# Kernel tuning notes

Hardware: AMD Instinct MI355X
Metric: run time of the kernel (lower is better)

The kernel has to match this reference:

```python
import jax, jax.numpy as jnp
import numpy as np

N = 50000   # nodes
E = 800000  # edges
D = 256     # input_dim == hidden_dim (required by original code path)
O = 32      # output_dim
ALPHA = 0.5      # APPNP teleport
ALPHA_RES = 0.0  # residual mix on output
BETA = 1.0       # neighbor-aggregation scale
EPS = 1e-12


def _l2norm(h):
    # F.normalize(h, p=2, dim=1)
    n = jnp.sqrt(jnp.sum(h * h, axis=1, keepdims=True))
    return h / jnp.maximum(n, EPS)


def _gappnp(x, row, col):
    # GAPPNP with K=1, symmetric normalization, self-loops (APPNP-style step)
    sl = jnp.arange(N, dtype=row.dtype)
    r = jnp.concatenate([row, sl])
    c = jnp.concatenate([col, sl])
    deg = jax.ops.segment_sum(jnp.ones(r.shape, x.dtype), r, num_segments=N)
    dinv = jnp.where(deg > 0, jax.lax.rsqrt(jnp.maximum(deg, 1.0)), 0.0)
    norm = dinv[r] * dinv[c]                      # [E+N]
    agg = jax.ops.segment_sum(norm[:, None] * x[c], r, num_segments=N)  # [N, D]
    h = (1.0 - ALPHA) * BETA * agg + ALPHA * x
    return (1.0 - ALPHA_RES) * h + ALPHA_RES * x


def setup_inputs() -> dict:
    key = jax.random.key(0)
    ks = jax.random.split(key, 8)
    s = 1.0 / np.sqrt(D)
    return {
        "x": jax.random.normal(ks[0], (N, D), dtype=jnp.float32),
        "edge_index": jax.random.randint(ks[1], (2, E), 0, N, dtype=jnp.int32),
        "W0": jax.random.normal(ks[2], (D, D), dtype=jnp.float32) * s,
        "b0": jnp.zeros((D,), jnp.float32),
        "Wn0": jax.random.normal(ks[3], (D, D), dtype=jnp.float32) * s,
        "bn0": jnp.zeros((D,), jnp.float32),
        "W1": jax.random.normal(ks[4], (D, D), dtype=jnp.float32) * s,
        "b1": jnp.zeros((D,), jnp.float32),
        "Wn1": jax.random.normal(ks[5], (D, D), dtype=jnp.float32) * s,
        "bn1": jnp.zeros((D,), jnp.float32),
        "W2": jax.random.normal(ks[6], (D, O), dtype=jnp.float32) * s,
        "b2": jnp.zeros((O,), jnp.float32),
    }


def reference(x, edge_index, W0, b0, Wn0, bn0, W1, b1, Wn1, bn1, W2, b2):
    # eval mode: dropout is identity
    row, col = edge_index[0], edge_index[1]
    h = x
    for (W, b, Wn, bn) in ((W0, b0, Wn0, bn0), (W1, b1, Wn1, bn1)):
        h = h @ W + b                       # fc[c]
        nb = h @ Wn + bn                    # fc_n[c] (separate_neighbors)
        nb = _gappnp(nb, row, col)          # propagate neighbors
        h = h + nb
        h = _l2norm(h)                      # norm == 'normalize'
        h = jax.nn.relu(h)                  # activation 'relu'
    h = h @ W2 + b2                         # final layer, no norm (c != 0)
    return h
```

## Files before the change

kernel.cpp:

```cpp
#include <hip/hip_runtime.h>
#include <hip/hip_bf16.h>

#define NN 50000
#define NE 800000
#define DD 256
#define OO 32
#define EB 3125
#define CASTB 12500
#define BCAP 64

typedef __attribute__((ext_vector_type(8))) short short8;
typedef __attribute__((ext_vector_type(4))) float float4v;

#define AS1 __attribute__((address_space(1)))
#define AS3 __attribute__((address_space(3)))

__device__ __forceinline__ float lo16f(unsigned int u) {
    union { unsigned int i; float f; } x; x.i = u << 16; return x.f;
}
__device__ __forceinline__ float hi16f(unsigned int u) {
    union { unsigned int i; float f; } x; x.i = u & 0xFFFF0000u; return x.f;
}
__device__ __forceinline__ unsigned short f2b(float f) {
    union { float f; unsigned int i; } x;
    x.f = f;
    unsigned int r = x.i + 0x7FFFu + ((x.i >> 16) & 1u);
    return (unsigned short)(r >> 16);
}

__device__ __forceinline__ int pack_idx(int k, int n) {
    return (k >> 5) * 8192 + (n >> 4) * 512 + (((k & 31) >> 3) * 16 + (n & 15)) * 8 + (k & 7);
}

__global__ __launch_bounds__(256) void pre_all(const int* __restrict__ row,
                                               const int* __restrict__ col,
                                               int* __restrict__ cnt,
                                               unsigned short* __restrict__ bucket,
                                               const float* __restrict__ x,
                                               unsigned short* __restrict__ xb,
                                               const float* __restrict__ W0,
                                               const float* __restrict__ Wn0,
                                               const float* __restrict__ W1,
                                               const float* __restrict__ Wn1,
                                               const float* __restrict__ W2,
                                               const float* __restrict__ b0_,
                                               const float* __restrict__ bn0,
                                               const float* __restrict__ b1_,
                                               const float* __restrict__ bn1,
                                               unsigned short* __restrict__ Wp0,
                                               unsigned short* __restrict__ Wp1,
                                               unsigned short* __restrict__ Wt2,
                                               float* __restrict__ bc0,
                                               float* __restrict__ bc1) {
    __shared__ float wrow[256];
    int b = blockIdx.x, t = threadIdx.x;
    if (b < EB) {
        int e = b * 256 + t;
        int r = row[e], c = col[e];
        int p = atomicAdd(&cnt[r], 1);
        if (p < BCAP) bucket[(size_t)r * BCAP + p] = (unsigned short)c;
    } else if (b < EB + 256) {
        int n = b - EB;
        Wp0[pack_idx(t, n)] = f2b(W0[t * 256 + n]);
    } else if (b < EB + 512) {
        int n = b - (EB + 256);
        Wp1[pack_idx(t, n)] = f2b(W1[t * 256 + n]);
    } else if (b < EB + 544) {
        int n = b - (EB + 512);
        Wt2[n * 256 + t] = f2b(W2[t * 32 + n]);
    } else if (b < EB + 800) {
        int k = b - (EB + 544);
        wrow[t] = W0[k * 256 + t];
        __syncthreads();
        float s = 0.f;
#pragma unroll 8
        for (int m = 0; m < 256; ++m) s = fmaf(wrow[m], Wn0[m * 256 + t], s);
        Wp0[pack_idx(k + 256, t)] = f2b(s);
    } else if (b < EB + 1056) {
        int k = b - (EB + 800);
        wrow[t] = W1[k * 256 + t];
        __syncthreads();
        float s = 0.f;
#pragma unroll 8
        for (int m = 0; m < 256; ++m) s = fmaf(wrow[m], Wn1[m * 256 + t], s);
        Wp1[pack_idx(k + 256, t)] = f2b(s);
    } else if (b == EB + 1056) {
        float s0 = bn0[t], s1 = bn1[t];
        for (int m = 0; m < 256; ++m) {
            s0 = fmaf(b0_[m], Wn0[m * 256 + t], s0);
            s1 = fmaf(b1_[m], Wn1[m * 256 + t], s1);
        }
        bc0[t] = s0;
        bc1[t] = s1;
    } else {
        int i = (b - (EB + 1057)) * 256 + t;
        float4 v = ((const float4*)x)[i];
        ushort4 o;
        o.x = f2b(v.x); o.y = f2b(v.y); o.z = f2b(v.z); o.w = f2b(v.w);
        ((ushort4*)xb)[i] = o;
    }
}

__global__ __launch_bounds__(256) void agg_g(const unsigned short* __restrict__ A,
                                             const int* __restrict__ cnt,
                                             const unsigned short* __restrict__ bucket,
                                             unsigned short* __restrict__ G,
                                             float* __restrict__ pv) {
    int wave = threadIdx.x >> 6, lane = threadIdx.x & 63;
    int half = lane >> 5, s = lane & 31;
    int v = blockIdx.x * 4 + wave;
    const uint4* A4 = (const uint4*)A;

    int deg = cnt[v];
    float dv = rsqrtf((float)(deg + 1));
    if (deg > BCAP) deg = BCAP;

    int c = 0;
    float dc = 0.f;
    if (lane < deg) {
        c = bucket[(size_t)v * BCAP + lane];
        dc = rsqrtf((float)(cnt[c] + 1));
    }
    float sdc = dc;

    float a0 = 0.f, a1 = 0.f, a2 = 0.f, a3 = 0.f;
    float a4 = 0.f, a5 = 0.f, a6 = 0.f, a7 = 0.f;

    int pairs4 = (((deg + 1) >> 1) + 3) & ~3;
    for (int j = 0; j < pairs4; j += 4) {
        int ci[4];
        float di[4];
        uint4 u[4];
#pragma unroll
        for (int q = 0; q < 4; ++q) {
            int srcl = 2 * (j + q) + half;
            ci[q] = __shfl(c, srcl);
            di[q] = __shfl(dc, srcl);
        }
#pragma unroll
        for (int q = 0; q < 4; ++q) u[q] = A4[(size_t)ci[q] * 32 + s];
#pragma unroll
        for (int q = 0; q < 4; ++q) {
            a0 = fmaf(di[q], lo16f(u[q].x), a0);
            a1 = fmaf(di[q], hi16f(u[q].x), a1);
            a2 = fmaf(di[q], lo16f(u[q].y), a2);
            a3 = fmaf(di[q], hi16f(u[q].y), a3);
            a4 = fmaf(di[q], lo16f(u[q].z), a4);
            a5 = fmaf(di[q], hi16f(u[q].z), a5);
            a6 = fmaf(di[q], lo16f(u[q].w), a6);
            a7 = fmaf(di[q], hi16f(u[q].w), a7);
        }
    }

    a0 += __shfl_xor(a0, 32); a1 += __shfl_xor(a1, 32);
    a2 += __shfl_xor(a2, 32); a3 += __shfl_xor(a3, 32);
    a4 += __shfl_xor(a4, 32); a5 += __shfl_xor(a5, 32);
    a6 += __shfl_xor(a6, 32); a7 += __shfl_xor(a7, 32);
#pragma unroll
    for (int o = 32; o > 0; o >>= 1) sdc += __shfl_xor(sdc, o);

    if (half == 0) {
        uint4 au = A4[(size_t)v * 32 + s];
        float av[8] = {lo16f(au.x), hi16f(au.x), lo16f(au.y), hi16f(au.y),
                       lo16f(au.z), hi16f(au.z), lo16f(au.w), hi16f(au.w)};
        float aa[8] = {a0, a1, a2, a3, a4, a5, a6, a7};
        unsigned short ov[8];
#pragma unroll
        for (int i = 0; i < 8; ++i)
            ov[i] = f2b(0.5f * dv * (dv * av[i] + aa[i]) + 0.5f * av[i]);
        *(short8*)&G[(size_t)v * 256 + s * 8] = *(short8*)ov;
    }
    if (lane == 0) pv[v] = 0.5f * dv * (dv + sdc) + 0.5f;
}

__global__ __launch_bounds__(256, 2) void gemm512_norm(const unsigned short* __restrict__ A,
                                                       const unsigned short* __restrict__ G,
                                                       const unsigned short* __restrict__ Wp,
                                                       const float* __restrict__ bias,
                                                       const float* __restrict__ biasc,
                                                       const float* __restrict__ pv,
                                                       unsigned short* __restrict__ Out,
                                                       int M) {
    __shared__ unsigned short smem[16384];
    int tid = threadIdx.x, lane = tid & 63, wave = tid >> 6;
    int fr = lane & 15, quad = lane >> 4, fk = quad * 8;
    int rb = blockIdx.x * 128;

    int r0 = rb + wave * 32 + fr;      if (r0 >= M) r0 = M - 1;
    int r1 = rb + wave * 32 + 16 + fr; if (r1 >= M) r1 = M - 1;
    const unsigned short* ap0 = A + (size_t)r0 * 256 + fk;
    const unsigned short* ap1 = A + (size_t)r1 * 256 + fk;
    const unsigned short* gp0 = G + (size_t)r0 * 256 + fk;
    const unsigned short* gp1 = G + (size_t)r1 * 256 + fk;

    float4v acc[2][16];
#pragma unroll
    for (int i = 0; i < 2; ++i)
#pragma unroll
        for (int j = 0; j < 16; ++j) acc[i][j] = (float4v){0.f, 0.f, 0.f, 0.f};

#pragma unroll
    for (int i = 0; i < 4; ++i) {
        int ch = wave * 4 + i;
        __builtin_amdgcn_global_load_lds((const AS1 void*)(Wp + ch * 512 + lane * 8),
                                         (AS3 void*)&smem[ch * 512], 16, 0, 0);
    }
    short8 a0c = *(const short8*)ap0;
    short8 a1c = *(const short8*)ap1;

    for (int kk = 0; kk < 16; ++kk) {
        __syncthreads();
        int cur = (kk & 1) * 8192;
        if (kk < 15) {
            int nxt = ((kk + 1) & 1) * 8192;
#pragma unroll
            for (int i = 0; i < 4; ++i) {
                int ch = wave * 4 + i;
                __builtin_amdgcn_global_load_lds(
                    (const AS1 void*)(Wp + (kk + 1) * 8192 + ch * 512 + lane * 8),
                    (AS3 void*)&smem[nxt + ch * 512], 16, 0, 0);
            }
        }
        short8 a0n, a1n;
        if (kk < 15) {
            int kn = kk + 1;
            a0n = (kn < 8) ? *(const short8*)(ap0 + kn * 32) : *(const short8*)(gp0 + (kn - 8) * 32);
            a1n = (kn < 8) ? *(const short8*)(ap1 + kn * 32) : *(const short8*)(gp1 + (kn - 8) * 32);
        }
#pragma unroll
        for (int j = 0; j < 16; ++j) {
            short8 b = *(const short8*)&smem[cur + j * 512 + lane * 8];
            acc[0][j] = __builtin_amdgcn_mfma_f32_16x16x32_bf16(a0c, b, acc[0][j], 0, 0, 0);
            acc[1][j] = __builtin_amdgcn_mfma_f32_16x16x32_bf16(a1c, b, acc[1][j], 0, 0, 0);
        }
        a0c = a0n;
        a1c = a1n;
    }

    float bv[16], bcv[16];
#pragma unroll
    for (int j = 0; j < 16; ++j) {
        bv[j] = bias[j * 16 + fr];
        bcv[j] = biasc[j * 16 + fr];
    }
    float pvr[2][4];
#pragma unroll
    for (int i = 0; i < 2; ++i)
#pragma unroll
        for (int r = 0; r < 4; ++r) {
            int rg = rb + wave * 32 + i * 16 + quad * 4 + r;
            if (rg >= M) rg = M - 1;
            pvr[i][r] = pv[rg];
        }
    float ss[2][4] = {{0.f, 0.f, 0.f, 0.f}, {0.f, 0.f, 0.f, 0.f}};
#pragma unroll
    for (int i = 0; i < 2; ++i)
#pragma unroll
        for (int j = 0; j < 16; ++j)
#pragma unroll
            for (int r = 0; r < 4; ++r) {
                float t = acc[i][j][r] + bv[j] + pvr[i][r] * bcv[j];
                acc[i][j][r] = t;
                ss[i][r] = fmaf(t, t, ss[i][r]);
            }
#pragma unroll
    for (int o = 1; o < 16; o <<= 1)
#pragma unroll
        for (int i = 0; i < 2; ++i)
#pragma unroll
            for (int r = 0; r < 4; ++r) ss[i][r] += __shfl_xor(ss[i][r], o);
    float inv[2][4];
#pragma unroll
    for (int i = 0; i < 2; ++i)
#pragma unroll
        for (int r = 0; r < 4; ++r) inv[i][r] = 1.0f / fmaxf(sqrtf(ss[i][r]), 1e-12f);

#pragma unroll
    for (int rd = 0; rd < 2; ++rd) {
        __syncthreads();
        if ((wave >> 1) == rd) {
#pragma unroll
            for (int i = 0; i < 2; ++i)
#pragma unroll
                for (int j = 0; j < 16; ++j)
#pragma unroll
                    for (int r = 0; r < 4; ++r)
                        smem[((wave & 1) * 32 + i * 16 + quad * 4 + r) * 256 + j * 16 + fr] =
                            f2b(fmaxf(acc[i][j][r] * inv[i][r], 0.f));
        }
        __syncthreads();
#pragma unroll
        for (int b = 0; b < 8; ++b) {
            int chunk = b * 256 + tid;
            int rw = chunk >> 5, part = chunk & 31;
            int gr = rb + rd * 64 + rw;
            if (gr < M)
                *(short8*)&Out[(size_t)gr * 256 + part * 8] =
                    *(const short8*)&smem[rw * 256 + part * 8];
        }
    }
}

__global__ __launch_bounds__(256) void gemm_final_mfma(const unsigned short* __restrict__ A,
                                                       const unsigned short* __restrict__ Wt2,
                                                       const float* __restrict__ b2,
                                                       float* __restrict__ out, int M) {
    __shared__ unsigned short Als[128 * 32];
    __shared__ unsigned short Bls[32 * 32];
    int tid = threadIdx.x;
    int lane = tid & 63, wave = tid >> 6;
    int rowBase = blockIdx.x * 128;

    float4v acc[2][2];
#pragma unroll
    for (int i = 0; i < 2; ++i)
#pragma unroll
        for (int j = 0; j < 2; ++j) acc[i][j] = (float4v){0.f, 0.f, 0.f, 0.f};

    int sRow = wave * 32 + (lane >> 2);
    int sK = (lane & 3) * 8;
    int fr = lane & 15, fk = (lane >> 4) * 8;
    int bn = tid >> 3, bk4 = (tid & 7) * 4;

    for (int k0 = 0; k0 < 256; k0 += 32) {
        int r0 = rowBase + sRow;       if (r0 >= M) r0 = M - 1;
        int r1 = rowBase + sRow + 16;  if (r1 >= M) r1 = M - 1;
        __builtin_amdgcn_global_load_lds((const AS1 void*)(A + (size_t)r0 * 256 + k0 + sK),
                                         (AS3 void*)&Als[(wave * 32) * 32], 16, 0, 0);
        __builtin_amdgcn_global_load_lds((const AS1 void*)(A + (size_t)r1 * 256 + k0 + sK),
                                         (AS3 void*)&Als[(wave * 32 + 16) * 32], 16, 0, 0);
        *(ushort4*)&Bls[bn * 32 + bk4] = *(const ushort4*)&Wt2[bn * 256 + k0 + bk4];
        __syncthreads();

        short8 af[2], bfr[2];
#pragma unroll
        for (int i = 0; i < 2; ++i)
            af[i] = *(const short8*)&Als[(wave * 32 + i * 16 + fr) * 32 + fk];
#pragma unroll
        for (int j = 0; j < 2; ++j)
            bfr[j] = *(const short8*)&Bls[(j * 16 + fr) * 32 + fk];
#pragma unroll
        for (int i = 0; i < 2; ++i)
#pragma unroll
            for (int j = 0; j < 2; ++j)
                acc[i][j] = __builtin_amdgcn_mfma_f32_16x16x32_bf16(af[i], bfr[j], acc[i][j], 0, 0, 0);
        __syncthreads();
    }

    int cr = (lane >> 4) * 4, cc = lane & 15;
#pragma unroll
    for (int i = 0; i < 2; ++i) {
#pragma unroll
        for (int j = 0; j < 2; ++j) {
            int colg = j * 16 + cc;
            float bv = b2[colg];
#pragma unroll
            for (int r = 0; r < 4; ++r) {
                int rowg = rowBase + wave * 32 + i * 16 + cr + r;
                if (rowg < M) out[(size_t)rowg * 32 + colg] = acc[i][j][r] + bv;
            }
        }
    }
}

extern "C" void kernel_launch(void* const* d_in, const int* in_sizes, int n_in,
                              void* d_out, int out_size, void* d_ws, size_t ws_size,
                              hipStream_t stream) {
    const float* x   = (const float*)d_in[0];
    const int* edge  = (const int*)d_in[1];
    const float* W0  = (const float*)d_in[2];
    const float* b0  = (const float*)d_in[3];
    const float* Wn0 = (const float*)d_in[4];
    const float* bn0 = (const float*)d_in[5];
    const float* W1  = (const float*)d_in[6];
    const float* b1  = (const float*)d_in[7];
    const float* Wn1 = (const float*)d_in[8];
    const float* bn1 = (const float*)d_in[9];
    const float* W2  = (const float*)d_in[10];
    const float* b2  = (const float*)d_in[11];
    float* out = (float*)d_out;

    const int N = NN, E = NE;
    const int* row = edge;
    const int* col = edge + E;

    char* p = (char*)d_ws;
    unsigned short* Xbf = (unsigned short*)p; p += (size_t)N * DD * 2;
    unsigned short* Gbf = (unsigned short*)p; p += (size_t)N * DD * 2;
    unsigned short* Abf = (unsigned short*)p; p += (size_t)N * DD * 2;
    unsigned short* Wp0 = (unsigned short*)p; p += 16 * 8192 * 2;
    unsigned short* Wp1 = (unsigned short*)p; p += 16 * 8192 * 2;
    unsigned short* Wt2 = (unsigned short*)p; p += 32 * 256 * 2;
    float* bc0   = (float*)p; p += 256 * 4;
    float* bc1   = (float*)p; p += 256 * 4;
    float* pv    = (float*)p; p += (size_t)N * 4;
    int* cnt     = (int*)p; p += (size_t)N * 4;
    unsigned short* bucket = (unsigned short*)p; p += (size_t)N * BCAP * 2;

    hipMemsetAsync(cnt, 0, (size_t)N * sizeof(int), stream);

    pre_all<<<EB + 1057 + CASTB, 256, 0, stream>>>(row, col, cnt, bucket, x, Xbf,
                                                   W0, Wn0, W1, Wn1, W2,
                                                   b0, bn0, b1, bn1,
                                                   Wp0, Wp1, Wt2, bc0, bc1);

    const int gTiles = (N + 127) / 128;
    agg_g<<<N / 4, 256, 0, stream>>>(Xbf, cnt, bucket, Gbf, pv);
    gemm512_norm<<<gTiles, 256, 0, stream>>>(Xbf, Gbf, Wp0, b0, bc0, pv, Abf, N);
    agg_g<<<N / 4, 256, 0, stream>>>(Abf, cnt, bucket, Gbf, pv);
    gemm512_norm<<<gTiles, 256, 0, stream>>>(Abf, Gbf, Wp1, b1, bc1, pv, Xbf, N);
    gemm_final_mfma<<<(N + 127) / 128, 256, 0, stream>>>(Xbf, Wt2, b2, out, N);
}
```

Measured before the change: 325.2 us.

## Fuse final output projection into second GEMM epilogue; vectorize edge bucketing

The final 256x32 projection is computed inside the second gemm512_norm epilogue. It uses the normalized tile already held in shared memory plus a swizzled LDS copy of Wt2, so the layer-2 activations are never written to and reread from global memory and one kernel launch is dropped. The edge-bucketing blocks now each process two edges per thread using int2 loads, which halves that block count. The cost is extra LDS use (16 KB for Wt2) and more epilogue work in the templated kernel, which could reduce occupancy.

```diff
diff --git a/kernel.cpp b/kernel.cpp
--- a/kernel.cpp
+++ b/kernel.cpp
@@ -5,7 +5,7 @@
 #define NE 800000
 #define DD 256
 #define OO 32
-#define EB 3125
+#define EB2 1563
 #define CASTB 12500
 #define BCAP 64
 
@@ -54,37 +54,42 @@
                                                float* __restrict__ bc1) {
     __shared__ float wrow[256];
     int b = blockIdx.x, t = threadIdx.x;
-    if (b < EB) {
-        int e = b * 256 + t;
-        int r = row[e], c = col[e];
-        int p = atomicAdd(&cnt[r], 1);
-        if (p < BCAP) bucket[(size_t)r * BCAP + p] = (unsigned short)c;
-    } else if (b < EB + 256) {
-        int n = b - EB;
+    if (b < EB2) {
+        int i = b * 256 + t;
+        if (i < NE / 2) {
+            int2 r2 = ((const int2*)row)[i];
+            int2 c2 = ((const int2*)col)[i];
+            int p0 = atomicAdd(&cnt[r2.x], 1);
+            if (p0 < BCAP) bucket[(size_t)r2.x * BCAP + p0] = (unsigned short)c2.x;
+            int p1 = atomicAdd(&cnt[r2.y], 1);
+            if (p1 < BCAP) bucket[(size_t)r2.y * BCAP + p1] = (unsigned short)c2.y;
+        }
+    } else if (b < EB2 + 256) {
+        int n = b - EB2;
         Wp0[pack_idx(t, n)] = f2b(W0[t * 256 + n]);
-    } else if (b < EB + 512) {
-        int n = b - (EB + 256);
+    } else if (b < EB2 + 512) {
+        int n = b - (EB2 + 256);
         Wp1[pack_idx(t, n)] = f2b(W1[t * 256 + n]);
-    } else if (b < EB + 544) {
-        int n = b - (EB + 512);
+    } else if (b < EB2 + 544) {
+        int n = b - (EB2 + 512);
         Wt2[n * 256 + t] = f2b(W2[t * 32 + n]);
-    } else if (b < EB + 800) {
-        int k = b - (EB + 544);
+    } else if (b < EB2 + 800) {
+        int k = b - (EB2 + 544);
         wrow[t] = W0[k * 256 + t];
         __syncthreads();
         float s = 0.f;
 #pragma unroll 8
         for (int m = 0; m < 256; ++m) s = fmaf(wrow[m], Wn0[m * 256 + t], s);
         Wp0[pack_idx(k + 256, t)] = f2b(s);
-    } else if (b < EB + 1056) {
-        int k = b - (EB + 800);
+    } else if (b < EB2 + 1056) {
+        int k = b - (EB2 + 800);
         wrow[t] = W1[k * 256 + t];
         __syncthreads();
         float s = 0.f;
 #pragma unroll 8
         for (int m = 0; m < 256; ++m) s = fmaf(wrow[m], Wn1[m * 256 + t], s);
         Wp1[pack_idx(k + 256, t)] = f2b(s);
-    } else if (b == EB + 1056) {
+    } else if (b == EB2 + 1056) {
         float s0 = bn0[t], s1 = bn1[t];
         for (int m = 0; m < 256; ++m) {
             s0 = fmaf(b0_[m], Wn0[m * 256 + t], s0);
@@ -93,7 +98,7 @@
         bc0[t] = s0;
         bc1[t] = s1;
     } else {
-        int i = (b - (EB + 1057)) * 256 + t;
+        int i = (b - (EB2 + 1057)) * 256 + t;
         float4 v = ((const float4*)x)[i];
         ushort4 o;
         o.x = f2b(v.x); o.y = f2b(v.y); o.z = f2b(v.z); o.w = f2b(v.w);
@@ -173,6 +178,7 @@
     if (lane == 0) pv[v] = 0.5f * dv * (dv + sdc) + 0.5f;
 }
 
+template <int FINAL>
 __global__ __launch_bounds__(256, 2) void gemm512_norm(const unsigned short* __restrict__ A,
                                                        const unsigned short* __restrict__ G,
                                                        const unsigned short* __restrict__ Wp,
@@ -180,8 +186,12 @@
                                                        const float* __restrict__ biasc,
                                                        const float* __restrict__ pv,
                                                        unsigned short* __restrict__ Out,
+                                                       const unsigned short* __restrict__ Wt2,
+                                                       const float* __restrict__ b2,
+                                                       float* __restrict__ outF,
                                                        int M) {
     __shared__ unsigned short smem[16384];
+    __shared__ unsigned short wt2ls[FINAL ? 8192 : 16];
     int tid = threadIdx.x, lane = tid & 63, wave = tid >> 6;
     int fr = lane & 15, quad = lane >> 4, fk = quad * 8;
     int rb = blockIdx.x * 128;
@@ -237,6 +247,16 @@
         a1c = a1n;
     }
 
+    if (FINAL) {
+#pragma unroll
+        for (int c = 0; c < 4; ++c) {
+            int idx = tid * 4 + c;
+            int n = idx >> 5, ch = idx & 31;
+            *(short8*)&wt2ls[n * 256 + ((ch ^ (n & 7)) << 3)] =
+                *(const short8*)&Wt2[n * 256 + ch * 8];
+        }
+    }
+
     float bv[16], bcv[16];
 #pragma unroll
     for (int j = 0; j < 16; ++j) {
@@ -284,80 +304,53 @@
 #pragma unroll
                 for (int j = 0; j < 16; ++j)
 #pragma unroll
-                    for (int r = 0; r < 4; ++r)
-                        smem[((wave & 1) * 32 + i * 16 + quad * 4 + r) * 256 + j * 16 + fr] =
-                            f2b(fmaxf(acc[i][j][r] * inv[i][r], 0.f));
+                    for (int r = 0; r < 4; ++r) {
+                        int rw = (wave & 1) * 32 + i * 16 + quad * 4 + r;
+                        unsigned short hv = f2b(fmaxf(acc[i][j][r] * inv[i][r], 0.f));
+                        if (FINAL) {
+                            int e = j * 16 + fr;
+                            smem[rw * 256 + (((e >> 3) ^ (rw & 7)) << 3) + (e & 7)] = hv;
+                        } else {
+                            smem[rw * 256 + j * 16 + fr] = hv;
+                        }
+                    }
         }
         __syncthreads();
-#pragma unroll
-        for (int b = 0; b < 8; ++b) {
-            int chunk = b * 256 + tid;
-            int rw = chunk >> 5, part = chunk & 31;
-            int gr = rb + rd * 64 + rw;
-            if (gr < M)
-                *(short8*)&Out[(size_t)gr * 256 + part * 8] =
-                    *(const short8*)&smem[rw * 256 + part * 8];
-        }
-    }
-}
-
-__global__ __launch_bounds__(256) void gemm_final_mfma(const unsigned short* __restrict__ A,
-                                                       const unsigned short* __restrict__ Wt2,
-                                                       const float* __restrict__ b2,
-                                                       float* __restrict__ out, int M) {
-    __shared__ unsigned short Als[128 * 32];
-    __shared__ unsigned short Bls[32 * 32];
-    int tid = threadIdx.x;
-    int lane = tid & 63, wave = tid >> 6;
-    int rowBase = blockIdx.x * 128;
-
-    float4v acc[2][2];
-#pragma unroll
-    for (int i = 0; i < 2; ++i)
-#pragma unroll
-        for (int j = 0; j < 2; ++j) acc[i][j] = (float4v){0.f, 0.f, 0.f, 0.f};
-
-    int sRow = wave * 32 + (lane >> 2);
-    int sK = (lane & 3) * 8;
-    int fr = lane & 15, fk = (lane >> 4) * 8;
-    int bn = tid >> 3, bk4 = (tid & 7) * 4;
-
-    for (int k0 = 0; k0 < 256; k0 += 32) {
-        int r0 = rowBase + sRow;       if (r0 >= M) r0 = M - 1;
-        int r1 = rowBase + sRow + 16;  if (r1 >= M) r1 = M - 1;
-        __builtin_amdgcn_global_load_lds((const AS1 void*)(A + (size_t)r0 * 256 + k0 + sK),
-                                         (AS3 void*)&Als[(wave * 32) * 32], 16, 0, 0);
-        __builtin_amdgcn_global_load_lds((const AS1 void*)(A + (size_t)r1 * 256 + k0 + sK),
-                                         (AS3 void*)&Als[(wave * 32 + 16) * 32], 16, 0, 0);
-        *(ushort4*)&Bls[bn * 32 + bk4] = *(const ushort4*)&Wt2[bn * 256 + k0 + bk4];
-        __syncthreads();
-
-        short8 af[2], bfr[2];
-#pragma unroll
-        for (int i = 0; i < 2; ++i)
-            af[i] = *(const short8*)&Als[(wave * 32 + i * 16 + fr) * 32 + fk];
-#pragma unroll
-        for (int j = 0; j < 2; ++j)
-            bfr[j] = *(const short8*)&Bls[(j * 16 + fr) * 32 + fk];
-#pragma unroll
-        for (int i = 0; i < 2; ++i)
-#pragma unroll
-            for (int j = 0; j < 2; ++j)
-                acc[i][j] = __builtin_amdgcn_mfma_f32_16x16x32_bf16(af[i], bfr[j], acc[i][j], 0, 0, 0);
-        __syncthreads();
-    }
-
-    int cr = (lane >> 4) * 4, cc = lane & 15;
-#pragma unroll
-    for (int i = 0; i < 2; ++i) {
-#pragma unroll
-        for (int j = 0; j < 2; ++j) {
-            int colg = j * 16 + cc;
-            float bv = b2[colg];
-#pragma unroll
-            for (int r = 0; r < 4; ++r) {
-                int rowg = rowBase + wave * 32 + i * 16 + cr + r;
-                if (rowg < M) out[(size_t)rowg * 32 + colg] = acc[i][j][r] + bv;
+        if (FINAL) {
+            float4v a2[2];
+            a2[0] = (float4v){0.f, 0.f, 0.f, 0.f};
+            a2[1] = (float4v){0.f, 0.f, 0.f, 0.f};
+            int hrow = wave * 16 + fr;
+#pragma unroll
+            for (int kk = 0; kk < 8; ++kk) {
+                int chb = kk * 4 + quad;
+                short8 af = *(const short8*)&smem[hrow * 256 + ((chb ^ (hrow & 7)) << 3)];
+#pragma unroll
+                for (int j = 0; j < 2; ++j) {
+                    int n = j * 16 + fr;
+                    short8 bf = *(const short8*)&wt2ls[n * 256 + ((chb ^ (n & 7)) << 3)];
+                    a2[j] = __builtin_amdgcn_mfma_f32_16x16x32_bf16(af, bf, a2[j], 0, 0, 0);
+                }
+            }
+#pragma unroll
+            for (int j = 0; j < 2; ++j) {
+                int colg = j * 16 + fr;
+                float bb = b2[colg];
+#pragma unroll
+                for (int r = 0; r < 4; ++r) {
+                    int gr = rb + rd * 64 + wave * 16 + quad * 4 + r;
+                    if (gr < M) outF[(size_t)gr * 32 + colg] = a2[j][r] + bb;
+                }
+            }
+        } else {
+#pragma unroll
+            for (int b = 0; b < 8; ++b) {
+                int chunk = b * 256 + tid;
+                int rw = chunk >> 5, part = chunk & 31;
+                int gr = rb + rd * 64 + rw;
+                if (gr < M)
+                    *(short8*)&Out[(size_t)gr * 256 + part * 8] =
+                        *(const short8*)&smem[rw * 256 + part * 8];
             }
         }
     }
@@ -399,15 +392,16 @@
 
     hipMemsetAsync(cnt, 0, (size_t)N * sizeof(int), stream);
 
-    pre_all<<<EB + 1057 + CASTB, 256, 0, stream>>>(row, col, cnt, bucket, x, Xbf,
-                                                   W0, Wn0, W1, Wn1, W2,
-                                                   b0, bn0, b1, bn1,
-                                                   Wp0, Wp1, Wt2, bc0, bc1);
+    pre_all<<<EB2 + 1057 + CASTB, 256, 0, stream>>>(row, col, cnt, bucket, x, Xbf,
+                                                    W0, Wn0, W1, Wn1, W2,
+                                                    b0, bn0, b1, bn1,
+                                                    Wp0, Wp1, Wt2, bc0, bc1);
 
     const int gTiles = (N + 127) / 128;
     agg_g<<<N / 4, 256, 0, stream>>>(Xbf, cnt, bucket, Gbf, pv);
-    gemm512_norm<<<gTiles, 256, 0, stream>>>(Xbf, Gbf, Wp0, b0, bc0, pv, Abf, N);
+    gemm512_norm<0><<<gTiles, 256, 0, stream>>>(Xbf, Gbf, Wp0, b0, bc0, pv, Abf,
+                                                Wt2, b2, out, N);
     agg_g<<<N / 4, 256, 0, stream>>>(Abf, cnt, bucket, Gbf, pv);
-    gemm512_norm<<<gTiles, 256, 0, stream>>>(Abf, Gbf, Wp1, b1, bc1, pv, Xbf, N);
-    gemm_final_mfma<<<(N + 127) / 128, 256, 0, stream>>>(Xbf, Wt2, b2, out, N);
-}
+    gemm512_norm<1><<<gTiles, 256, 0, stream>>>(Abf, Gbf, Wp1, b1, bc1, pv, Xbf,
+                                                Wt2, b2, out, N);
+}
```

After: 333.6 us. +2.6%, slower.
